# Kernel optimization log

Hardware: AMD Instinct MI355X
Metric: run time of the kernel (lower is better)

Reference implementation:

```python
import jax, jax.numpy as jnp
import numpy as np

B, S, D, H = 2, 2048, 1024, 16
HD = D // H
SCALING = HD ** -0.5


def _length_mask(lengths, seqlen):
    return (jnp.arange(seqlen)[None, :] < jnp.asarray(lengths)[:, None]).astype(jnp.int32)


def setup_inputs() -> dict:
    key = jax.random.key(0)
    ks = jax.random.split(key, 10)
    std = D ** -0.5
    inp = {
        "hidden_states": jax.random.normal(ks[0], (B, S, D), dtype=jnp.float32),
        "Wq": jax.random.normal(ks[1], (D, D), dtype=jnp.float32) * std,
        "bq": jax.random.normal(ks[2], (D,), dtype=jnp.float32) * 0.02,
        "Wk": jax.random.normal(ks[3], (D, D), dtype=jnp.float32) * std,
        "bk": jax.random.normal(ks[4], (D,), dtype=jnp.float32) * 0.02,
        "Wv": jax.random.normal(ks[5], (D, D), dtype=jnp.float32) * std,
        "bv": jax.random.normal(ks[6], (D,), dtype=jnp.float32) * 0.02,
        "Wo": jax.random.normal(ks[7], (D, D), dtype=jnp.float32) * std,
        "bo": jax.random.normal(ks[8], (D,), dtype=jnp.float32) * 0.02,
        # variable valid lengths per batch element (padding at the end)
        "query_mask_1d": _length_mask([S, S - 512], S),
        "key_mask_1d": _length_mask([S, S - 512], S),
    }
    return inp


def reference(hidden_states, Wq, bq, Wk, bk, Wv, bv, Wo, bo, query_mask_1d, key_mask_1d):
    bsz, tgt_len, _ = hidden_states.shape
    # projections (dropout p=0 / eval -> identity)
    q = (hidden_states @ Wq + bq) * SCALING
    k = hidden_states @ Wk + bk
    v = hidden_states @ Wv + bv
    q = q.reshape(bsz, tgt_len, H, HD).transpose(0, 2, 1, 3)  # [B,H,S,HD]
    k = k.reshape(bsz, -1, H, HD).transpose(0, 2, 1, 3)
    v = v.reshape(bsz, -1, H, HD).transpose(0, 2, 1, 3)

    scores = jnp.einsum("bhqd,bhkd->bhqk", q, k)  # [B,H,S,S]
    q_valid = (query_mask_1d != 0)[:, None, :, None]  # [B,1,S,1]
    k_valid = (key_mask_1d != 0)[:, None, None, :]    # [B,1,1,S]
    # masked_fill(-inf) on padded keys; padded-query rows would be all -inf ->
    # softmax NaN -> nan_to_num(0). We compute the same result NaN-free by
    # zeroing the scores of padded-query rows and zeroing their probs after.
    s = jnp.where(k_valid, scores, -jnp.inf)
    s = jnp.where(q_valid, s, 0.0)
    attn_weights = jax.nn.softmax(s, axis=-1) * q_valid  # == softmax + nan_to_num

    attn_output = jnp.einsum("bhqk,bhkd->bhqd", attn_weights, v)
    attn_output = attn_output.transpose(0, 2, 1, 3).reshape(bsz, tgt_len, D)
    attn_output = attn_output @ Wo + bo
    return attn_output
```

## Files before the change

kernel.cpp:

```cpp
#include <hip/hip_runtime.h>
#include <stdint.h>

#define BB 2
#define SS 2048
#define DD 1024
#define HH 16
#define HDIM 64
#define MTOT (BB*SS)
#define QK_SCALE_LOG2E 0.180336880f

typedef unsigned short u16;
typedef __attribute__((ext_vector_type(8))) __bf16 bf16x8;
typedef __attribute__((ext_vector_type(4))) float f32x4;

static __device__ __forceinline__ float exp2_hw(float x) {
    return __builtin_amdgcn_exp2f(x);
}

static __device__ __forceinline__ u16 f2bu(float f) {
    union { float f; uint32_t u; } c; c.f = f;
    uint32_t u = c.u + 0x7fffu + ((c.u >> 16) & 1u);
    return (u16)(u >> 16);
}

static __device__ __forceinline__ u16 f2b_hw(float f) {
    __bf16 b = (__bf16)f;
    union { __bf16 b; u16 u; } c; c.b = b;
    return c.u;
}

static __device__ __forceinline__ uint32_t cvt_pk_bf16(float lo, float hi) {
    uint32_t r;
    asm("v_cvt_pk_bf16_f32 %0, %1, %2" : "=v"(r) : "v"(lo), "v"(hi));
    return r;
}

static __device__ __forceinline__ void gload_lds16(const void* g, void* l) {
    __builtin_amdgcn_global_load_lds(
        (const __attribute__((address_space(1))) uint32_t*)(g),
        (__attribute__((address_space(3))) uint32_t*)(l),
        16, 0, 0);
}

__global__ void k_convert_x(const float* __restrict__ x, u16* __restrict__ xb) {
    int i = (blockIdx.x * blockDim.x + threadIdx.x) * 4;
    float4 v = *(const float4*)(x + i);
    ushort4 o;
    o.x = f2bu(v.x); o.y = f2bu(v.y); o.z = f2bu(v.z); o.w = f2bu(v.w);
    *(ushort4*)(xb + i) = o;
}

__global__ void k_transpose_w(const float* __restrict__ Wq, const float* __restrict__ Wk,
                              const float* __restrict__ Wv, const float* __restrict__ Wo,
                              u16* __restrict__ Wqkv_t, u16* __restrict__ Wo_t) {
    __shared__ float tile[32][33];
    const int which = blockIdx.z;
    const float* W = (which == 0) ? Wq : (which == 1) ? Wk : (which == 2) ? Wv : Wo;
    u16* dst = (which < 3) ? (Wqkv_t + (size_t)which * DD * DD) : Wo_t;
    const int n0 = blockIdx.x * 32, k0 = blockIdx.y * 32;
    const int tx = threadIdx.x, ty = threadIdx.y;
    #pragma unroll
    for (int i = 0; i < 32; i += 8)
        tile[ty + i][tx] = W[(size_t)(k0 + ty + i) * DD + (n0 + tx)];
    __syncthreads();
    #pragma unroll
    for (int i = 0; i < 32; i += 8)
        dst[(size_t)(n0 + ty + i) * DD + (k0 + tx)] = f2bu(tile[tx][ty + i]);
}

#define PH_BODY(BUF, Q, READB, STAGECODE, TAILWAIT)                           \
  { bf16x8 afr[2][2];                                                         \
    _Pragma("unroll") for (int m2 = 0; m2 < 2; ++m2)                          \
      _Pragma("unroll") for (int ks = 0; ks < 2; ++ks)                        \
        afr[m2][ks] = rdA(BUF, 2*(Q)+m2, ks);                                 \
    if (READB) {                                                              \
      _Pragma("unroll") for (int nf = 0; nf < 4; ++nf)                        \
        _Pragma("unroll") for (int ks = 0; ks < 2; ++ks)                      \
          bfr[nf][ks] = rdB(BUF, nf, ks);                                     \
    }                                                                         \
    STAGECODE;                                                                \
    __builtin_amdgcn_s_barrier();                                             \
    asm volatile("s_waitcnt lgkmcnt(0)" ::: "memory");                        \
    __builtin_amdgcn_sched_barrier(0);                                        \
    __builtin_amdgcn_s_setprio(1);                                            \
    _Pragma("unroll") for (int m2 = 0; m2 < 2; ++m2)                          \
      _Pragma("unroll") for (int nf = 0; nf < 4; ++nf)                        \
        _Pragma("unroll") for (int ks = 0; ks < 2; ++ks)                      \
          acc[2*(Q)+m2][nf] = __builtin_amdgcn_mfma_f32_16x16x32_bf16(        \
              afr[m2][ks], bfr[nf][ks], acc[2*(Q)+m2][nf], 0, 0, 0);          \
    __builtin_amdgcn_s_setprio(0);                                            \
    TAILWAIT;                                                                 \
    __builtin_amdgcn_s_barrier();                                             \
  }

__global__ __launch_bounds__(512, 2) void k_gemm_qkv(
    const u16* __restrict__ Xb, const u16* __restrict__ Wt,
    const float* __restrict__ bq, const float* __restrict__ bk_, const float* __restrict__ bv,
    u16* __restrict__ Qb, u16* __restrict__ Kb, u16* __restrict__ Vt)
{
    __shared__ u16 As[2][256 * 64];
    __shared__ u16 Bs[2][256 * 64];

    const int flat = blockIdx.y * 12 + blockIdx.x;
    const int swz = (flat & 7) * 24 + (flat >> 3);
    const int bx = swz % 12, by = swz / 12;
    const int m0 = by << 8, n0 = bx << 8;

    const int t = threadIdx.x;
    const int lane = t & 63, w = t >> 6;
    const int wm = (w >> 2) << 7, wn = (w & 3) << 6;
    const int lr = lane & 15, lg = lane >> 4;

    const u16* Asrc = Xb + (size_t)m0 * DD;
    const u16* Bsrc = Wt + (size_t)n0 * DD;

    f32x4 acc[8][4] = {};
    bf16x8 bfr[4][2];

    auto stgA = [&](int buf, int half, int tt) {
        #pragma unroll
        for (int r = 0; r < 2; ++r) {
            int off = (t + (r << 9)) << 4;
            int row = off >> 7, colb = off & 127;
            int scol = colb ^ ((row & 7) << 4);
            gload_lds16(Asrc + (size_t)((half << 7) + row) * DD + (tt << 6) + (scol >> 1),
                        (char*)As[buf] + (half << 14) + off);
        }
    };
    auto stgB = [&](int buf, int half, int tt) {
        #pragma unroll
        for (int r = 0; r < 2; ++r) {
            int off = (t + (r << 9)) << 4;
            int row = off >> 7, colb = off & 127;
            int scol = colb ^ ((row & 7) << 4);
            gload_lds16(Bsrc + (size_t)((half << 7) + row) * DD + (tt << 6) + (scol >> 1),
                        (char*)Bs[buf] + (half << 14) + off);
        }
    };

    auto rdA = [&](int buf, int mf, int ks) {
        const int row = wm + (mf << 4) + lr;
        const int col = ((ks << 6) + (lg << 4)) ^ ((row & 7) << 4);
        return *(const bf16x8*)((const char*)As[buf] + row * 128 + col);
    };
    auto rdB = [&](int buf, int nf, int ks) {
        const int row = wn + (nf << 4) + lr;
        const int col = ((ks << 6) + (lg << 4)) ^ ((row & 7) << 4);
        return *(const bf16x8*)((const char*)Bs[buf] + row * 128 + col);
    };

    stgA(0, 0, 0); stgA(0, 1, 0); stgB(0, 0, 0); stgB(0, 1, 0);
    stgB(1, 0, 1); stgB(1, 1, 1);
    asm volatile("s_waitcnt vmcnt(4)" ::: "memory");
    __builtin_amdgcn_s_barrier();

    #pragma unroll 1
    for (int i = 0; i < 7; ++i) {
        const int t1 = 2 * i + 1, t2 = 2 * i + 2, t3 = 2 * i + 3;
        PH_BODY(0, 0, true,  { stgA(1, 0, t1); }, {});
        PH_BODY(0, 1, false, { stgA(1, 1, t1); }, {});
        PH_BODY(0, 2, false, { stgB(0, 0, t2); }, {});
        PH_BODY(0, 3, false, { stgB(0, 1, t2); },
                { asm volatile("s_waitcnt vmcnt(4)" ::: "memory"); });
        PH_BODY(1, 0, true,  { stgA(0, 0, t2); }, {});
        PH_BODY(1, 1, false, { stgA(0, 1, t2); }, {});
        PH_BODY(1, 2, false, { stgB(1, 0, t3); }, {});
        PH_BODY(1, 3, false, { stgB(1, 1, t3); },
                { asm volatile("s_waitcnt vmcnt(4)" ::: "memory"); });
    }
    PH_BODY(0, 0, true,  { stgA(1, 0, 15); }, {});
    PH_BODY(0, 1, false, { stgA(1, 1, 15); }, {});
    PH_BODY(0, 2, false, {}, {});
    PH_BODY(0, 3, false, {},
            { asm volatile("s_waitcnt vmcnt(0)" ::: "memory"); });
    PH_BODY(1, 0, true,  {}, {});
    PH_BODY(1, 1, false, {}, {});
    PH_BODY(1, 2, false, {}, {});
    PH_BODY(1, 3, false, {}, {});

    const int which = n0 >> 10;
    #pragma unroll
    for (int mf = 0; mf < 8; ++mf) {
        #pragma unroll
        for (int nf = 0; nf < 4; ++nf) {
            const int n = n0 + wn + (nf << 4) + lr;
            const int mbase = m0 + wm + (mf << 4) + (lg << 2);
            const int b_ = mbase >> 11;
            const int s_ = mbase & 2047;
            const int nn = n & 1023;
            const int hh = nn >> 6, d = nn & 63;
            if (which == 0) {
                const float bias = bq[nn];
                u16* dstp = Qb + (((size_t)b_ * HH + hh) * SS + s_) * HDIM + d;
                #pragma unroll
                for (int r = 0; r < 4; ++r)
                    dstp[(size_t)r * HDIM] = f2bu((acc[mf][nf][r] + bias) * QK_SCALE_LOG2E);
            } else if (which == 1) {
                const float bias = bk_[nn];
                u16* dstp = Kb + (((size_t)b_ * HH + hh) * SS + s_) * HDIM + d;
                #pragma unroll
                for (int r = 0; r < 4; ++r)
                    dstp[(size_t)r * HDIM] = f2bu(acc[mf][nf][r] + bias);
            } else {
                const float bias = bv[nn];
                ushort4 pk;
                pk.x = f2bu(acc[mf][nf][0] + bias);
                pk.y = f2bu(acc[mf][nf][1] + bias);
                pk.z = f2bu(acc[mf][nf][2] + bias);
                pk.w = f2bu(acc[mf][nf][3] + bias);
                *(ushort4*)(Vt + (((size_t)b_ * HH + hh) * HDIM + d) * SS + s_) = pk;
            }
        }
    }
}

__global__ __launch_bounds__(256) void k_attn(
    const u16* __restrict__ Qb, const u16* __restrict__ Kb, const u16* __restrict__ Vt,
    const int* __restrict__ qmask, const int* __restrict__ kmask,
    u16* __restrict__ X2)
{
    const int blk = blockIdx.x;
    const int qt = blk & 31;
    const int h = (blk >> 5) & 15;
    const int b_ = blk >> 9;
    const int t = threadIdx.x;
    const int lane = t & 63, w = t >> 6;
    const int lr = lane & 15, lg = lane >> 4;

    __shared__ u16 Ks[2][64 * 64];
    __shared__ u16 Vs[2][64 * 64];
    __shared__ u16 Ps[4][16 * 64];

    const int q0 = qt << 6;
    const size_t bh = (size_t)b_ * HH + h;
    const u16* Qbase = Qb + bh * SS * HDIM;
    const char* KbaseB = (const char*)(Kb + bh * SS * HDIM);
    const char* VbaseB = (const char*)(Vt + bh * HDIM * SS);

    if (qmask[b_ * SS + q0] == 0) {
        #pragma unroll
        for (int r = 0; r < 4; ++r) {
            const int q = q0 + (w << 4) + (lg << 2) + r;
            #pragma unroll
            for (int nf = 0; nf < 4; ++nf)
                X2[((size_t)b_ * SS + q) * DD + (h << 6) + (nf << 4) + lr] = 0;
        }
        return;
    }

    int kv = (lane < 32) ? kmask[b_ * SS + (lane << 6)] : 0;
    unsigned long long bal = __ballot(kv != 0);
    const int nkt = __popcll(bal);

    bf16x8 qf[2];
    #pragma unroll
    for (int ks = 0; ks < 2; ++ks)
        qf[ks] = *(const bf16x8*)(Qbase + (size_t)(q0 + (w << 4) + lr) * HDIM + (ks << 5) + (lg << 3));

    bf16x8 vones;
    #pragma unroll
    for (int i = 0; i < 8; ++i) vones[i] = (__bf16)1.0f;

    f32x4 o[4] = {};
    f32x4 lacc = {};

    auto stage = [&](int buf, int kb) {
        #pragma unroll
        for (int i = 0; i < 2; ++i) {
            int off = (t + (i << 8)) << 4;
            int row = off >> 7, colb = off & 127;
            int scol = colb ^ ((row & 7) << 4);
            gload_lds16(KbaseB + (size_t)(kb + row) * 128 + scol, (char*)Ks[buf] + off);
            gload_lds16(VbaseB + ((size_t)row * SS + (size_t)kb) * 2 + scol, (char*)Vs[buf] + off);
        }
    };

    if (nkt > 0) stage(0, 0);
    __syncthreads();

    u16* P = Ps[w];

    int cur = 0;
    for (int kt = 0; kt < nkt; ++kt) {
        const int kb = kt << 6;
        if (kt + 1 < nkt) stage(cur ^ 1, kb + 64);

        f32x4 sf[4] = {};
        #pragma unroll
        for (int ks = 0; ks < 2; ++ks) {
            #pragma unroll
            for (int f = 0; f < 4; ++f) {
                const int krow = (f << 4) + lr;
                const int kcol = ((ks << 6) + (lg << 4)) ^ ((krow & 7) << 4);
                bf16x8 kf = *(const bf16x8*)((const char*)Ks[cur] + krow * 128 + kcol);
                sf[f] = __builtin_amdgcn_mfma_f32_16x16x32_bf16(kf, qf[ks], sf[f], 0, 0, 0);
            }
        }
        if (kt == nkt - 1) {
            #pragma unroll
            for (int f = 0; f < 4; ++f) {
                #pragma unroll
                for (int r = 0; r < 4; ++r) {
                    if (kmask[b_ * SS + kb + (f << 4) + (lg << 2) + r] == 0)
                        sf[f][r] = -1e30f;
                }
            }
        }
        #pragma unroll
        for (int f = 0; f < 4; ++f)
            #pragma unroll
            for (int r = 0; r < 4; ++r)
                sf[f][r] = exp2_hw(sf[f][r]);

        #pragma unroll
        for (int f = 0; f < 4; ++f) {
            uint2 pk;
            pk.x = cvt_pk_bf16(sf[f][0], sf[f][1]);
            pk.y = cvt_pk_bf16(sf[f][2], sf[f][3]);
            *(uint2*)((char*)P + (((lr << 7) + (f << 5) + (lg << 3)) ^ ((lr & 7) << 4))) = pk;
        }

        #pragma unroll
        for (int ks = 0; ks < 2; ++ks) {
            bf16x8 pa = *(const bf16x8*)((const char*)P + (((lr << 7) + (ks << 6) + (lg << 4)) ^ ((lr & 7) << 4)));
            lacc = __builtin_amdgcn_mfma_f32_16x16x32_bf16(pa, vones, lacc, 0, 0, 0);
            #pragma unroll
            for (int nf = 0; nf < 4; ++nf) {
                const int vrow = (nf << 4) + lr;
                const int vcol = ((ks << 6) + (lg << 4)) ^ ((vrow & 7) << 4);
                bf16x8 vb = *(const bf16x8*)((const char*)Vs[cur] + vrow * 128 + vcol);
                o[nf] = __builtin_amdgcn_mfma_f32_16x16x32_bf16(pa, vb, o[nf], 0, 0, 0);
            }
        }
        __syncthreads();
        cur ^= 1;
    }

    #pragma unroll
    for (int r = 0; r < 4; ++r) {
        const int q = q0 + (w << 4) + (lg << 2) + r;
        float l = lacc[r];
        float inv = (l > 0.f) ? __builtin_amdgcn_rcpf(l) : 0.f;
        if (qmask[b_ * SS + q] == 0) inv = 0.f;
        #pragma unroll
        for (int nf = 0; nf < 4; ++nf)
            X2[((size_t)b_ * SS + q) * DD + (h << 6) + (nf << 4) + lr] = f2b_hw(o[nf][r] * inv);
    }
}

__global__ __launch_bounds__(256) void k_gemm_out(
    const u16* __restrict__ X2, const u16* __restrict__ Wot,
    const float* __restrict__ bo, float* __restrict__ out)
{
    __shared__ u16 As2[2][128 * 64];
    __shared__ u16 Bs2[2][128 * 64];
    const int m0 = blockIdx.y * 128, n0 = blockIdx.x * 128;
    const int t = threadIdx.x;
    const int lane = t & 63, w = t >> 6;
    const int wm = (w >> 1) << 6, wn = (w & 1) << 6;
    const int lr = lane & 15, lg = lane >> 4;

    f32x4 acc[4][4] = {};

    auto stage = [&](int buf, int k0) {
        #pragma unroll
        for (int i = 0; i < 4; ++i) {
            int off = (t + (i << 8)) << 4;
            int row = off >> 7, colb = off & 127;
            int scol = colb ^ ((row & 7) << 4);
            gload_lds16(X2 + (size_t)(m0 + row) * DD + k0 + (scol >> 1), (char*)As2[buf] + off);
            gload_lds16(Wot + (size_t)(n0 + row) * DD + k0 + (scol >> 1), (char*)Bs2[buf] + off);
        }
    };

    stage(0, 0);
    __syncthreads();

    int cur = 0;
    for (int kt = 0; kt < 16; ++kt) {
        if (kt < 15) stage(cur ^ 1, (kt + 1) << 6);
        #pragma unroll
        for (int ks = 0; ks < 2; ++ks) {
            bf16x8 a[4], b[4];
            #pragma unroll
            for (int i = 0; i < 4; ++i) {
                const int row = wm + (i << 4) + lr;
                a[i] = *(const bf16x8*)((const char*)As2[cur] + row * 128 + (((ks << 6) + (lg << 4)) ^ ((row & 7) << 4)));
            }
            #pragma unroll
            for (int i = 0; i < 4; ++i) {
                const int row = wn + (i << 4) + lr;
                b[i] = *(const bf16x8*)((const char*)Bs2[cur] + row * 128 + (((ks << 6) + (lg << 4)) ^ ((row & 7) << 4)));
            }
            #pragma unroll
            for (int mi = 0; mi < 4; ++mi)
                #pragma unroll
                for (int ni = 0; ni < 4; ++ni)
                    acc[mi][ni] = __builtin_amdgcn_mfma_f32_16x16x32_bf16(a[mi], b[ni], acc[mi][ni], 0, 0, 0);
        }
        __syncthreads();
        cur ^= 1;
    }

    #pragma unroll
    for (int mi = 0; mi < 4; ++mi) {
        #pragma unroll
        for (int ni = 0; ni < 4; ++ni) {
            const int n = n0 + wn + (ni << 4) + lr;
            const int mbase = m0 + wm + (mi << 4) + (lg << 2);
            const float bias = bo[n];
            #pragma unroll
            for (int r = 0; r < 4; ++r)
                out[(size_t)(mbase + r) * DD + n] = acc[mi][ni][r] + bias;
        }
    }
}

extern "C" void kernel_launch(void* const* d_in, const int* in_sizes, int n_in,
                              void* d_out, int out_size, void* d_ws, size_t ws_size,
                              hipStream_t stream) {
    const float* hs = (const float*)d_in[0];
    const float* Wq = (const float*)d_in[1];
    const float* bq = (const float*)d_in[2];
    const float* Wk = (const float*)d_in[3];
    const float* bk = (const float*)d_in[4];
    const float* Wv = (const float*)d_in[5];
    const float* bv = (const float*)d_in[6];
    const float* Wo = (const float*)d_in[7];
    const float* bo = (const float*)d_in[8];
    const int* qm = (const int*)d_in[9];
    const int* km = (const int*)d_in[10];
    float* out = (float*)d_out;

    char* ws = (char*)d_ws;
    const size_t MB = 1024 * 1024;
    u16* Xb  = (u16*)(ws + 0);
    u16* Wt3 = (u16*)(ws + 8 * MB);
    u16* Wot = (u16*)(ws + 14 * MB);
    u16* Qb  = (u16*)(ws + 16 * MB);
    u16* Kb  = (u16*)(ws + 24 * MB);
    u16* Vt  = (u16*)(ws + 32 * MB);
    u16* X2  = (u16*)(ws + 40 * MB);

    k_convert_x<<<dim3(MTOT * DD / 1024), dim3(256), 0, stream>>>(hs, Xb);
    k_transpose_w<<<dim3(32, 32, 4), dim3(32, 8), 0, stream>>>(Wq, Wk, Wv, Wo, Wt3, Wot);
    k_gemm_qkv<<<dim3(12, 16), dim3(512), 0, stream>>>(Xb, Wt3, bq, bk, bv, Qb, Kb, Vt);
    k_attn<<<dim3(1024), dim3(256), 0, stream>>>(Qb, Kb, Vt, qm, km, X2);
    k_gemm_out<<<dim3(8, 32), dim3(256), 0, stream>>>(X2, Wot, bo, out);
}
```

Measured before the change: 123.1 us.

## Restructure attention kernel: 128-query blocks, triple-buffered KV, XCD-aware grid mapping

The attention kernel now runs 512 threads (8 waves) per block covering 128 queries, so each staged K/V tile is shared by twice as many waves. K/V staging moves from double to triple buffering with prefetch two tiles ahead, using explicit vmcnt waits and raw barriers instead of __syncthreads. Block indices are remapped so that blocks of the same batch-head land on the same XCD, which should improve L2 reuse. MFMA sections are wrapped in s_setprio. The changes aim at global-load latency, barrier cost and redundant K/V traffic, at the cost of more LDS per block and possibly lower occupancy.

After: 117.0 us. -4.9%, faster.

```diff
diff --git a/kernel.cpp b/kernel.cpp
--- a/kernel.cpp
+++ b/kernel.cpp
@@ -214,28 +214,31 @@
     }
 }
 
-__global__ __launch_bounds__(256) void k_attn(
+__global__ __launch_bounds__(512, 4) void k_attn(
     const u16* __restrict__ Qb, const u16* __restrict__ Kb, const u16* __restrict__ Vt,
     const int* __restrict__ qmask, const int* __restrict__ kmask,
     u16* __restrict__ X2)
 {
-    const int blk = blockIdx.x;
-    const int qt = blk & 31;
-    const int h = (blk >> 5) & 15;
-    const int b_ = blk >> 9;
+    const int i = blockIdx.x;
+    const int xcd = i & 7, j = i >> 3;
+    const int qt = j & 15;
+    const int bh = xcd + ((j >> 4) << 3);
+    const int b_ = bh >> 4;
+    const int h = bh & 15;
+
     const int t = threadIdx.x;
     const int lane = t & 63, w = t >> 6;
     const int lr = lane & 15, lg = lane >> 4;
 
-    __shared__ u16 Ks[2][64 * 64];
-    __shared__ u16 Vs[2][64 * 64];
-    __shared__ u16 Ps[4][16 * 64];
-
-    const int q0 = qt << 6;
-    const size_t bh = (size_t)b_ * HH + h;
-    const u16* Qbase = Qb + bh * SS * HDIM;
-    const char* KbaseB = (const char*)(Kb + bh * SS * HDIM);
-    const char* VbaseB = (const char*)(Vt + bh * HDIM * SS);
+    __shared__ u16 Ks[3][64 * 64];
+    __shared__ u16 Vs[3][64 * 64];
+    __shared__ u16 Ps[8][16 * 64];
+
+    const int q0 = qt << 7;
+    const size_t bhs = (size_t)b_ * HH + h;
+    const u16* Qbase = Qb + bhs * SS * HDIM;
+    const char* KbaseB = (const char*)(Kb + bhs * SS * HDIM);
+    const char* VbaseB = (const char*)(Vt + bhs * HDIM * SS);
 
     if (qmask[b_ * SS + q0] == 0) {
         #pragma unroll
@@ -259,33 +262,38 @@
 
     bf16x8 vones;
     #pragma unroll
-    for (int i = 0; i < 8; ++i) vones[i] = (__bf16)1.0f;
+    for (int i2 = 0; i2 < 8; ++i2) vones[i2] = (__bf16)1.0f;
 
     f32x4 o[4] = {};
     f32x4 lacc = {};
 
     auto stage = [&](int buf, int kb) {
-        #pragma unroll
-        for (int i = 0; i < 2; ++i) {
-            int off = (t + (i << 8)) << 4;
-            int row = off >> 7, colb = off & 127;
-            int scol = colb ^ ((row & 7) << 4);
-            gload_lds16(KbaseB + (size_t)(kb + row) * 128 + scol, (char*)Ks[buf] + off);
-            gload_lds16(VbaseB + ((size_t)row * SS + (size_t)kb) * 2 + scol, (char*)Vs[buf] + off);
-        }
+        const int off = t << 4;
+        const int row = off >> 7, colb = off & 127;
+        const int scol = colb ^ ((row & 7) << 4);
+        gload_lds16(KbaseB + (size_t)(kb + row) * 128 + scol, (char*)Ks[buf] + off);
+        gload_lds16(VbaseB + ((size_t)row * SS + (size_t)kb) * 2 + scol, (char*)Vs[buf] + off);
     };
 
     if (nkt > 0) stage(0, 0);
-    __syncthreads();
+    if (nkt > 1) stage(1, 64);
+    if (nkt > 1) { asm volatile("s_waitcnt vmcnt(2)" ::: "memory"); }
+    else         { asm volatile("s_waitcnt vmcnt(0)" ::: "memory"); }
+    __builtin_amdgcn_sched_barrier(0);
+    __builtin_amdgcn_s_barrier();
 
     u16* P = Ps[w];
 
     int cur = 0;
+    #pragma unroll 1
     for (int kt = 0; kt < nkt; ++kt) {
         const int kb = kt << 6;
-        if (kt + 1 < nkt) stage(cur ^ 1, kb + 64);
+        const int nxt = (cur == 2) ? 0 : cur + 1;
+        const int nx2 = (nxt == 2) ? 0 : nxt + 1;
+        if (kt + 2 < nkt) stage(nx2, kb + 128);
 
         f32x4 sf[4] = {};
+        __builtin_amdgcn_s_setprio(1);
         #pragma unroll
         for (int ks = 0; ks < 2; ++ks) {
             #pragma unroll
@@ -296,6 +304,7 @@
                 sf[f] = __builtin_amdgcn_mfma_f32_16x16x32_bf16(kf, qf[ks], sf[f], 0, 0, 0);
             }
         }
+        __builtin_amdgcn_s_setprio(0);
         if (kt == nkt - 1) {
             #pragma unroll
             for (int f = 0; f < 4; ++f) {
@@ -320,6 +329,7 @@
             *(uint2*)((char*)P + (((lr << 7) + (f << 5) + (lg << 3)) ^ ((lr & 7) << 4))) = pk;
         }
 
+        __builtin_amdgcn_s_setprio(1);
         #pragma unroll
         for (int ks = 0; ks < 2; ++ks) {
             bf16x8 pa = *(const bf16x8*)((const char*)P + (((lr << 7) + (ks << 6) + (lg << 4)) ^ ((lr & 7) << 4)));
@@ -332,8 +342,13 @@
                 o[nf] = __builtin_amdgcn_mfma_f32_16x16x32_bf16(pa, vb, o[nf], 0, 0, 0);
             }
         }
-        __syncthreads();
-        cur ^= 1;
+        __builtin_amdgcn_s_setprio(0);
+
+        if (kt + 2 < nkt) { asm volatile("s_waitcnt vmcnt(2)" ::: "memory"); }
+        else              { asm volatile("s_waitcnt vmcnt(0)" ::: "memory"); }
+        __builtin_amdgcn_sched_barrier(0);
+        __builtin_amdgcn_s_barrier();
+        cur = nxt;
     }
 
     #pragma unroll
@@ -445,6 +460,6 @@
     k_convert_x<<<dim3(MTOT * DD / 1024), dim3(256), 0, stream>>>(hs, Xb);
     k_transpose_w<<<dim3(32, 32, 4), dim3(32, 8), 0, stream>>>(Wq, Wk, Wv, Wo, Wt3, Wot);
     k_gemm_qkv<<<dim3(12, 16), dim3(512), 0, stream>>>(Xb, Wt3, bq, bk, bv, Qb, Kb, Vt);
-    k_attn<<<dim3(1024), dim3(256), 0, stream>>>(Qb, Kb, Vt, qm, km, X2);
+    k_attn<<<dim3(512), dim3(512), 0, stream>>>(Qb, Kb, Vt, qm, km, X2);
     k_gemm_out<<<dim3(8, 32), dim3(256), 0, stream>>>(X2, Wot, bo, out);
 }
```
